# Performance work log

Measured on AMD Instinct MI355X. Metric: run time of the kernel, lower is better.

Reference implementation:

```python
import jax, jax.numpy as jnp
import numpy as np

# ---- constants from the module ----
E_L, E_e, E_i = -65.0, 0.0, -80.0
V_th, V_reset, V_floor = -50.0, -65.0, -200.0
dt = 0.25
T_STEPS = 4000
DECAY_AMPA = float(np.exp(-dt / 2.0))   # tau_ampa = 2.0
DECAY_GABA = float(np.exp(-dt / 9.0))   # tau_gaba = 9.0
C_M_E, G_L_E = 1.0, 1.0 / 20.0          # tau_m_E = 20
C_M_I, G_L_I = 0.5, 0.5 / 5.0           # tau_m_I = 5
REF_E = 12                               # round(3.0/0.25)
REF_I = 6                                # round(1.5/0.25)
CM_BACK = 80.0
SLOPE = 1.0                              # biophysical surrogate slope

@jax.custom_vjp
def spike(u):
    # Heaviside forward, fast-sigmoid surrogate backward (SurrogateSpike)
    return (u >= 0).astype(u.dtype)

def _spike_fwd(u):
    return (u >= 0).astype(u.dtype), u

def _spike_bwd(u, g):
    return (g * SLOPE / (1.0 + SLOPE * jnp.abs(u)) ** 2,)

spike.defvjp(_spike_fwd, _spike_bwd)

def _scale_grad(x, scale):
    # forward identity, gradient scaled by `scale`
    return x * scale + jax.lax.stop_gradient(x) * (1.0 - scale)

def lif_step(v, I_total, ref, C_m, g_L, ref_steps):
    dv = (dt / C_m) * (-g_L * (v - E_L) + I_total)
    dv = _scale_grad(dv, 1.0 / CM_BACK)
    v = jnp.maximum(v + dv, V_floor)
    ref = jnp.maximum(ref - 1, 0)
    can_spike = ref == 0
    s = spike(v - V_th) * can_spike.astype(v.dtype)
    spiked_or_ref = (s > 0) | ~can_spike
    v = jnp.where(spiked_or_ref, V_reset, v)
    ref = jnp.where(s > 0, ref_steps, ref)
    return v, s, ref

def setup_inputs() -> dict:
    key = jax.random.key(0)
    ks = jax.random.split(key, 6)
    T, B, N_IN, N_E, N_I, N_OUT = T_STEPS, 64, 64, 256, 64, 10

    def init_w(k, shape, mean, std):
        # init_weight: N(mean,std) clamped >=0, fan-in normalized
        w = jnp.maximum(jax.random.normal(k, shape, jnp.float32) * std + mean, 0.0)
        return w / shape[0]

    return {
        "input_spikes": (jax.random.uniform(ks[0], (T, B, N_IN)) < 0.02).astype(jnp.float32),
        "W_ff0": init_w(ks[1], (N_IN, N_E), 5.1, 3.8),
        "W_ff1": init_w(ks[2], (N_E, N_OUT), 5.1, 3.8),
        "W_ee": init_w(ks[3], (N_E, N_E), 0.0, 0.0),
        "W_ei": init_w(ks[4], (N_E, N_I), 1.0, 0.5),
        "W_ie": init_w(ks[5], (N_I, N_E), 3.0, 1.5),
    }

def reference(input_spikes, W_ff0, W_ff1, W_ee, W_ei, W_ie):
    # Dale's law: feedforward weights clamped >= 0 in forward
    W0 = jnp.maximum(W_ff0, 0.0)
    W1 = jnp.maximum(W_ff1, 0.0)
    B = input_spikes.shape[1]
    N_E, N_I, N_OUT = W0.shape[1], W_ei.shape[1], W1.shape[1]
    f32 = input_spikes.dtype

    z = lambda n: jnp.zeros((B, n), f32)
    vl = lambda n: jnp.full((B, n), E_L, f32)
    zr = lambda n: jnp.zeros((B, n), jnp.int32)

    carry0 = (vl(N_E), zr(N_E), z(N_E), z(N_E), z(N_E),   # E pop: v, ref, g_ampa, g_gaba, spikes
              vl(N_I), zr(N_I), z(N_I), z(N_I),           # I pop: v, ref, g_ampa, spikes
              vl(N_OUT), zr(N_OUT), z(N_OUT),             # out pop: v, ref, g_ampa
              z(N_OUT))                                    # output spike accumulator

    def step(c, s_in):
        v_e, r_e, ge_e, gi_e, s_e, v_i, r_i, ge_i, s_i, v_o, r_o, g_o, acc = c
        # exp_synapse: spike kicks first, then decay
        ge_e = (ge_e + s_in @ W0 + s_e @ W_ee) * DECAY_AMPA
        gi_e = (gi_e + s_i @ W_ie) * DECAY_GABA
        ge_i = (ge_i + s_e @ W_ei) * DECAY_AMPA
        # E neurons: COBA with excitation + inhibition
        v_e, s_e, r_e = lif_step(v_e, ge_e * (E_e - v_e) + gi_e * (E_i - v_e), r_e, C_M_E, G_L_E, REF_E)
        # I neurons: COBA excitation only
        v_i, s_i, r_i = lif_step(v_i, ge_i * (E_e - v_i), r_i, C_M_I, G_L_I, REF_I)
        # output layer driven by fresh E spikes
        g_o = (g_o + s_e @ W1) * DECAY_AMPA
        v_o, s_o, r_o = lif_step(v_o, g_o * (E_e - v_o), r_o, C_M_E, G_L_E, REF_E)
        acc = acc + s_o
        return (v_e, r_e, ge_e, gi_e, s_e, v_i, r_i, ge_i, s_i, v_o, r_o, g_o, acc), None

    cT, _ = jax.lax.scan(step, carry0, input_spikes)
    return cT[-1]  # [B, N_OUT] output spike counts over T_steps
```

## Files before the change

kernel.cpp:

```cpp
#include <hip/hip_runtime.h>
#include <math.h>

#pragma clang fp contract(off)

#define BB 64
#define N_IN 64
#define N_E 256
#define N_I 64
#define N_OUT 10

__device__ inline unsigned long long rfl64(unsigned long long x) {
  unsigned int lo = __builtin_amdgcn_readfirstlane((unsigned int)x);
  unsigned int hi = __builtin_amdgcn_readfirstlane((unsigned int)(x >> 32));
  return (((unsigned long long)hi) << 32) | (unsigned long long)lo;
}

__global__ __launch_bounds__(256, 1) void ping_kernel(
    const float* __restrict__ g_in,
    const float* __restrict__ g_W0,
    const float* __restrict__ g_W1,
    const float* __restrict__ g_Wee,
    const float* __restrict__ g_Wei,
    const float* __restrict__ g_Wie,
    float* __restrict__ g_out,
    int T, float dA, float dG)
{
  const int tid  = threadIdx.x;
  const int lane = tid & 63;
  const int wav  = tid >> 6;
  const int b    = blockIdx.x;
  const int col  = (lane < N_OUT) ? lane : 0;
  const int colO = 64 + col;

  __shared__ float sWie[N_I * N_E];
  __shared__ float sWeiO[N_E * 80];
  __shared__ float sZeroRow[256];
  __shared__ __align__(16) float sPK[2][64][4];
  __shared__ __align__(16) float sKoT[2][16][4];
  __shared__ __align__(16) unsigned sTag[2][4];
  __shared__ unsigned long long sME[2][4];
  __shared__ int sWee;

  {
    const float4* s0 = (const float4*)g_Wie; float4* d0 = (float4*)sWie;
    for (int k = tid; k < (N_I * N_E) / 4; k += 256) d0[k] = s0[k];
    {
      int j = tid;
      float* row = &sWeiO[j * 80];
      for (int c = 0; c < 64; ++c) row[c] = g_Wei[j * N_I + c];
      for (int o = 0; o < N_OUT; ++o) row[64 + o] = fmaxf(g_W1[j * N_OUT + o], 0.f);
      for (int c = 74; c < 80; ++c) row[c] = 0.f;
    }
  }
  sZeroRow[tid] = 0.f;
  if (tid < 4) { sME[0][tid] = 0ull; sME[1][tid] = 0ull; }
  if (tid < 8) sTag[tid >> 2][tid & 3] = 0u;
  if (tid == 0) sWee = 0;
  {
    bool any = false;
    const float4* p = (const float4*)g_Wee;
    for (int k = tid; k < (N_E * N_E) / 4; k += 256) {
      float4 x = p[k];
      any |= (x.x != 0.f) | (x.y != 0.f) | (x.z != 0.f) | (x.w != 0.f);
    }
    if (__ballot(any) != 0ull && lane == 0) sWee = 1;
  }
  __syncthreads();
  const int wee = sWee;

  float vE = -65.f, ge = 0.f, gi = 0.f; int rE = 0;
  float vI = -65.f, gI = 0.f; int rI = 0;
  float vO = -65.f, gO = 0.f, accO = 0.f; int rO = 0;

  unsigned long long mE = 0ull;
  unsigned long long mI = 0ull;

  float cur = g_in[b * N_IN + lane];
  float n1  = g_in[((T > 1 ? 1 : 0) * BB + b) * N_IN + lane];

  unsigned long long mInC = __ballot(cur != 0.f);
  unsigned long long aRemC = 0ull;
  bool vaC[4] = {false, false, false, false};
  float fwC[4];
  if (mInC) {
    unsigned long long a = mInC;
    int ja[4];
#pragma unroll
    for (int k = 0; k < 4; ++k) {
      vaC[k] = (a != 0ull); ja[k] = vaC[k] ? (__ffsll(a) - 1) : 0; a &= (a - 1ull);
    }
    aRemC = a;
#pragma unroll
    for (int k = 0; k < 4; ++k) fwC[k] = g_W0[ja[k] * N_E + tid];
  }

  const int base64 = wav * 64;

  if (!wee) {
    for (int t = 0; t < T; ++t) {
      const int slot = t & 1;
      const int tp = (t + 2 < T) ? (t + 2) : (T - 1);
      float n2 = g_in[(tp * BB + b) * N_IN + lane];

      float pEI = 0.f, kow = 0.f;
      {
        unsigned long long e = mE;
        while (e) {
          const float* qb[4];
#pragma unroll
          for (int k = 0; k < 4; ++k) {
            bool v = (e != 0ull); int j = v ? (__ffsll(e) - 1) : 0; e &= (e - 1ull);
            qb[k] = v ? &sWeiO[(base64 + j) * 80] : sZeroRow;
          }
          float fq[4], fr[4];
#pragma unroll
          for (int k = 0; k < 4; ++k) { fq[k] = qb[k][lane]; fr[k] = qb[k][colO]; }
#pragma unroll
          for (int k = 0; k < 4; ++k) pEI += fq[k];
#pragma unroll
          for (int k = 0; k < 4; ++k) kow += fr[k];
        }
      }

      sPK[slot][lane][wav] = pEI;
      if (lane < 16) sKoT[slot][lane][wav] = kow;
      asm volatile("" ::: "memory");
      if (lane == 0) *((volatile unsigned*)&sTag[slot][wav]) = (unsigned)(t + 1);

      unsigned long long pr0 = ((volatile unsigned long long*)&sTag[slot][0])[0];
      unsigned long long pr1 = ((volatile unsigned long long*)&sTag[slot][0])[1];

      float kie = 0.f;
      {
        unsigned long long c = mI;
        while (c) {
          const float* pb[8];
#pragma unroll
          for (int k = 0; k < 8; ++k) {
            bool v = (c != 0ull); int j = v ? (__ffsll(c) - 1) : 0; c &= (c - 1ull);
            pb[k] = v ? &sWie[j * N_E] : sZeroRow;
          }
          float fI[8];
#pragma unroll
          for (int k = 0; k < 8; ++k) fI[k] = pb[k][tid];
#pragma unroll
          for (int k = 0; k < 8; ++k) kie += fI[k];
        }
      }

      float kin = 0.f;
      if (mInC) {
#pragma unroll
        for (int k = 0; k < 4; ++k) kin += vaC[k] ? fmaxf(fwC[k], 0.f) : 0.f;
        while (aRemC) {
          int j = __ffsll(aRemC) - 1; aRemC &= (aRemC - 1ull);
          kin += fmaxf(g_W0[j * N_E + tid], 0.f);
        }
      }

      ge = (ge + kin) * dA;
      gi = (gi + kie) * dG;
      {
        float t2 = ge * (0.f - vE);
        float t3 = gi * (-80.f - vE);
        float Itot = t2 + t3;
        float dv = 0.25f * ((-0.05f) * (vE - (-65.f)) + Itot);
        dv = dv * 0.0125f + dv * 0.9875f;
        vE = fmaxf(vE + dv, -200.f);
        rE = rE - 1; if (rE < 0) rE = 0;
        bool can = (rE == 0);
        bool sE = ((vE - (-50.f)) >= 0.f) && can;
        vE = (sE || !can) ? -65.f : vE;
        rE = sE ? 12 : rE;
        mE = __ballot(sE);
      }

      mInC = __ballot(n1 != 0.f);
      aRemC = 0ull;
      vaC[0] = vaC[1] = vaC[2] = vaC[3] = false;
      if (mInC) {
        unsigned long long a = mInC;
        int ja[4];
#pragma unroll
        for (int k = 0; k < 4; ++k) {
          vaC[k] = (a != 0ull); ja[k] = vaC[k] ? (__ffsll(a) - 1) : 0; a &= (a - 1ull);
        }
        aRemC = a;
#pragma unroll
        for (int k = 0; k < 4; ++k) fwC[k] = g_W0[ja[k] * N_E + tid];
      }

      {
        const unsigned want = (unsigned)(t + 1);
        const unsigned long long want2 = (((unsigned long long)want) << 32) | want;
        if ((((pr0 ^ want2) | (pr1 ^ want2))) != 0ull) {
          volatile unsigned long long* vt = (volatile unsigned long long*)&sTag[slot][0];
          while (true) {
            unsigned long long a0 = vt[0], a1 = vt[1];
            if (((a0 ^ want2) | (a1 ^ want2)) == 0ull) break;
          }
        }
        asm volatile("" ::: "memory");
      }

      float4 P = *(const float4*)&sPK[slot][lane][0];
      float4 K = *(const float4*)&sKoT[slot][col][0];

      {
        float p = ((P.x + P.y) + P.z) + P.w;
        gI = (gI + p) * dA;
        float Ii = gI * (0.f - vI);
        float dvi = 0.5f * ((-0.1f) * (vI - (-65.f)) + Ii);
        dvi = dvi * 0.0125f + dvi * 0.9875f;
        vI = fmaxf(vI + dvi, -200.f);
        rI = rI - 1; if (rI < 0) rI = 0;
        bool canI = (rI == 0);
        bool sI = ((vI - (-50.f)) >= 0.f) && canI;
        vI = (sI || !canI) ? -65.f : vI;
        rI = sI ? 6 : rI;
        mI = __ballot(sI);
      }

      {
        float ko = ((K.x + K.y) + K.z) + K.w;
        gO = (gO + ko) * dA;
        float Io = gO * (0.f - vO);
        float dvo = 0.25f * ((-0.05f) * (vO - (-65.f)) + Io);
        dvo = dvo * 0.0125f + dvo * 0.9875f;
        vO = fmaxf(vO + dvo, -200.f);
        rO = rO - 1; if (rO < 0) rO = 0;
        bool canO = (rO == 0);
        bool sO = ((vO - (-50.f)) >= 0.f) && canO;
        vO = (sO || !canO) ? -65.f : vO;
        rO = sO ? 12 : rO;
        accO += sO ? 1.f : 0.f;
      }

      cur = n1; n1 = n2;
    }
  } else {
    unsigned long long we0 = 0ull, we1 = 0ull, we2 = 0ull, we3 = 0ull;
    for (int t = 0; t < T; ++t) {
      const int slot = t & 1;
      const int tp = (t + 2 < T) ? (t + 2) : (T - 1);
      float n2 = g_in[(tp * BB + b) * N_IN + lane];

      float pEI = 0.f, kow = 0.f;
      {
        unsigned long long e = mE;
        while (e) {
          const float* qb[4];
#pragma unroll
          for (int k = 0; k < 4; ++k) {
            bool v = (e != 0ull); int j = v ? (__ffsll(e) - 1) : 0; e &= (e - 1ull);
            qb[k] = v ? &sWeiO[(base64 + j) * 80] : sZeroRow;
          }
          float fq[4], fr[4];
#pragma unroll
          for (int k = 0; k < 4; ++k) { fq[k] = qb[k][lane]; fr[k] = qb[k][colO]; }
#pragma unroll
          for (int k = 0; k < 4; ++k) pEI += fq[k];
#pragma unroll
          for (int k = 0; k < 4; ++k) kow += fr[k];
        }
      }
      sPK[slot][lane][wav] = pEI;
      if (lane < 16) sKoT[slot][lane][wav] = kow;
      asm volatile("s_waitcnt lgkmcnt(0)" ::: "memory");
      if (lane == 0) *((volatile unsigned*)&sTag[slot][wav]) = (unsigned)(t + 1);

      float kie = 0.f;
      {
        unsigned long long c = mI;
        while (c) {
          const float* pb[8];
#pragma unroll
          for (int k = 0; k < 8; ++k) {
            bool v = (c != 0ull); int j = v ? (__ffsll(c) - 1) : 0; c &= (c - 1ull);
            pb[k] = v ? &sWie[j * N_E] : sZeroRow;
          }
          float fI[8];
#pragma unroll
          for (int k = 0; k < 8; ++k) fI[k] = pb[k][tid];
#pragma unroll
          for (int k = 0; k < 8; ++k) kie += fI[k];
        }
      }

      float kin = 0.f;
      if (mInC) {
#pragma unroll
        for (int k = 0; k < 4; ++k) kin += vaC[k] ? fmaxf(fwC[k], 0.f) : 0.f;
        while (aRemC) {
          int j = __ffsll(aRemC) - 1; aRemC &= (aRemC - 1ull);
          kin += fmaxf(g_W0[j * N_E + tid], 0.f);
        }
      }

      float kee = 0.f;
      {
        unsigned long long m0 = we0, m1 = we1, m2 = we2, m3 = we3;
        while (m0 | m1 | m2 | m3) {
          bool h0 = (m0 != 0ull), h1 = (m1 != 0ull), h2 = (m2 != 0ull), h3 = (m3 != 0ull);
          int idx = 0;
          if (h0)      { idx = __ffsll(m0) - 1;       m0 &= (m0 - 1ull); }
          else if (h1) { idx = 64 + __ffsll(m1) - 1;  m1 &= (m1 - 1ull); }
          else if (h2) { idx = 128 + __ffsll(m2) - 1; m2 &= (m2 - 1ull); }
          else if (h3) { idx = 192 + __ffsll(m3) - 1; m3 &= (m3 - 1ull); }
          kee += g_Wee[idx * N_E + tid];
        }
      }

      ge = ((ge + kin) + kee) * dA;
      gi = (gi + kie) * dG;
      {
        float t2 = ge * (0.f - vE);
        float t3 = gi * (-80.f - vE);
        float Itot = t2 + t3;
        float dv = 0.25f * ((-0.05f) * (vE - (-65.f)) + Itot);
        dv = dv * 0.0125f + dv * 0.9875f;
        vE = fmaxf(vE + dv, -200.f);
        rE = rE - 1; if (rE < 0) rE = 0;
        bool can = (rE == 0);
        bool sE = ((vE - (-50.f)) >= 0.f) && can;
        vE = (sE || !can) ? -65.f : vE;
        rE = sE ? 12 : rE;
        unsigned long long fresh = __ballot(sE);
        if (lane == 0) sME[slot][wav] = fresh;
        mE = fresh;
      }

      mInC = __ballot(n1 != 0.f);
      aRemC = 0ull;
      vaC[0] = vaC[1] = vaC[2] = vaC[3] = false;
      if (mInC) {
        unsigned long long a = mInC;
        int ja[4];
#pragma unroll
        for (int k = 0; k < 4; ++k) {
          vaC[k] = (a != 0ull); ja[k] = vaC[k] ? (__ffsll(a) - 1) : 0; a &= (a - 1ull);
        }
        aRemC = a;
#pragma unroll
        for (int k = 0; k < 4; ++k) fwC[k] = g_W0[ja[k] * N_E + tid];
      }

      {
        const unsigned want = (unsigned)(t + 1);
        const unsigned long long want2 = (((unsigned long long)want) << 32) | want;
        volatile unsigned long long* vt = (volatile unsigned long long*)&sTag[slot][0];
        while (true) {
          unsigned long long a0 = vt[0], a1 = vt[1];
          if (((a0 ^ want2) | (a1 ^ want2)) == 0ull) break;
        }
        asm volatile("" ::: "memory");
      }

      float4 P = *(const float4*)&sPK[slot][lane][0];
      float4 K = *(const float4*)&sKoT[slot][col][0];

      {
        float p = ((P.x + P.y) + P.z) + P.w;
        gI = (gI + p) * dA;
        float Ii = gI * (0.f - vI);
        float dvi = 0.5f * ((-0.1f) * (vI - (-65.f)) + Ii);
        dvi = dvi * 0.0125f + dvi * 0.9875f;
        vI = fmaxf(vI + dvi, -200.f);
        rI = rI - 1; if (rI < 0) rI = 0;
        bool canI = (rI == 0);
        bool sI = ((vI - (-50.f)) >= 0.f) && canI;
        vI = (sI || !canI) ? -65.f : vI;
        rI = sI ? 6 : rI;
        mI = __ballot(sI);
      }

      {
        float ko = ((K.x + K.y) + K.z) + K.w;
        gO = (gO + ko) * dA;
        float Io = gO * (0.f - vO);
        float dvo = 0.25f * ((-0.05f) * (vO - (-65.f)) + Io);
        dvo = dvo * 0.0125f + dvo * 0.9875f;
        vO = fmaxf(vO + dvo, -200.f);
        rO = rO - 1; if (rO < 0) rO = 0;
        bool canO = (rO == 0);
        bool sO = ((vO - (-50.f)) >= 0.f) && canO;
        vO = (sO || !canO) ? -65.f : vO;
        rO = sO ? 12 : rO;
        accO += sO ? 1.f : 0.f;
      }

      __syncthreads();
      we0 = rfl64(sME[slot][0]); we1 = rfl64(sME[slot][1]);
      we2 = rfl64(sME[slot][2]); we3 = rfl64(sME[slot][3]);

      cur = n1; n1 = n2;
    }
  }

  {
    float kd = 0.f;
    unsigned long long e = mE;
    while (e) {
      const float* rb[4];
#pragma unroll
      for (int k = 0; k < 4; ++k) {
        bool v = (e != 0ull); int j = v ? (__ffsll(e) - 1) : 0; e &= (e - 1ull);
        rb[k] = v ? &sWeiO[(base64 + j) * 80] : sZeroRow;
      }
      float fr[4];
#pragma unroll
      for (int k = 0; k < 4; ++k) fr[k] = rb[k][colO];
#pragma unroll
      for (int k = 0; k < 4; ++k) kd += fr[k];
    }
    __syncthreads();
    if (lane < 16) sKoT[0][lane][wav] = kd;
    __syncthreads();
    float4 K = *(const float4*)&sKoT[0][col][0];
    float ko = ((K.x + K.y) + K.z) + K.w;
    gO = (gO + ko) * dA;
    float Io = gO * (0.f - vO);
    float dvo = 0.25f * ((-0.05f) * (vO - (-65.f)) + Io);
    dvo = dvo * 0.0125f + dvo * 0.9875f;
    vO = fmaxf(vO + dvo, -200.f);
    rO = rO - 1; if (rO < 0) rO = 0;
    bool canO = (rO == 0);
    bool sO = ((vO - (-50.f)) >= 0.f) && canO;
    accO += sO ? 1.f : 0.f;
  }

  if (wav == 0 && lane < N_OUT) g_out[b * N_OUT + lane] = accO;
}

extern "C" void kernel_launch(void* const* d_in, const int* in_sizes, int n_in,
                              void* d_out, int out_size, void* d_ws, size_t ws_size,
                              hipStream_t stream) {
  const float* g_in  = (const float*)d_in[0];
  const float* g_W0  = (const float*)d_in[1];
  const float* g_W1  = (const float*)d_in[2];
  const float* g_Wee = (const float*)d_in[3];
  const float* g_Wei = (const float*)d_in[4];
  const float* g_Wie = (const float*)d_in[5];
  float* out = (float*)d_out;
  int T = in_sizes[0] / (BB * N_IN);
  float dA = (float)exp(-0.25 / 2.0);
  float dG = (float)exp(-0.25 / 9.0);
  ping_kernel<<<dim3(BB), dim3(256), 0, stream>>>(g_in, g_W0, g_W1, g_Wee, g_Wei, g_Wie, out, T, dA, dG);
}
```

Baseline: 4.770 ms.

## Add dedicated fifth wave for I/output populations to pipeline recurrence

Launches 320 threads and moves the inhibitory and output population updates (in the W_ee==0 path) onto a fifth wavefront. It exchanges spike masks with the four E-neuron waves through shared-memory tagged slots, so the E and I updates of consecutive timesteps can overlap instead of serializing in one wave. The change also widens the E-spike gather unroll from 4 to 8 and vectorizes the weight staging loads. The cost is extra spin-wait handshakes between waves and one more wave per block.

Result: no change. 4.745 ms (median of 2 runs) (-0.5%).

```diff
diff --git a/kernel.cpp b/kernel.cpp
--- a/kernel.cpp
+++ b/kernel.cpp
@@ -15,7 +15,7 @@
   return (((unsigned long long)hi) << 32) | (unsigned long long)lo;
 }
 
-__global__ __launch_bounds__(256, 1) void ping_kernel(
+__global__ __launch_bounds__(320, 1) void ping_kernel(
     const float* __restrict__ g_in,
     const float* __restrict__ g_W0,
     const float* __restrict__ g_W1,
@@ -31,6 +31,7 @@
   const int b    = blockIdx.x;
   const int col  = (lane < N_OUT) ? lane : 0;
   const int colO = 64 + col;
+  const int base64 = wav * 64;
 
   __shared__ float sWie[N_I * N_E];
   __shared__ float sWeiO[N_E * 80];
@@ -38,398 +39,468 @@
   __shared__ __align__(16) float sPK[2][64][4];
   __shared__ __align__(16) float sKoT[2][16][4];
   __shared__ __align__(16) unsigned sTag[2][4];
+  __shared__ __align__(8) unsigned long long sMI[2];
+  __shared__ unsigned sMITag[2];
   __shared__ unsigned long long sME[2][4];
   __shared__ int sWee;
 
   {
     const float4* s0 = (const float4*)g_Wie; float4* d0 = (float4*)sWie;
-    for (int k = tid; k < (N_I * N_E) / 4; k += 256) d0[k] = s0[k];
-    {
-      int j = tid;
-      float* row = &sWeiO[j * 80];
-      for (int c = 0; c < 64; ++c) row[c] = g_Wei[j * N_I + c];
-      for (int o = 0; o < N_OUT; ++o) row[64 + o] = fmaxf(g_W1[j * N_OUT + o], 0.f);
-      for (int c = 74; c < 80; ++c) row[c] = 0.f;
-    }
+    for (int k = tid; k < (N_I * N_E) / 4; k += 320) d0[k] = s0[k];
+    const float4* wei4 = (const float4*)g_Wei;
+    for (int k = tid; k < 256 * 16; k += 320) {
+      int r = k >> 4, c4 = k & 15;
+      *(float4*)&sWeiO[r * 80 + c4 * 4] = wei4[k];
+    }
+    for (int k = tid; k < 256 * N_OUT; k += 320) {
+      int r = k / N_OUT, o = k - r * N_OUT;
+      sWeiO[r * 80 + 64 + o] = fmaxf(g_W1[k], 0.f);
+    }
+    for (int k = tid; k < 256 * 6; k += 320) {
+      int r = k / 6, c = k - r * 6;
+      sWeiO[r * 80 + 74 + c] = 0.f;
+    }
+    for (int k = tid; k < 256; k += 320) sZeroRow[k] = 0.f;
   }
-  sZeroRow[tid] = 0.f;
-  if (tid < 4) { sME[0][tid] = 0ull; sME[1][tid] = 0ull; }
   if (tid < 8) sTag[tid >> 2][tid & 3] = 0u;
+  if (tid < 8) sME[tid >> 2][tid & 3] = 0ull;
+  if (tid < 2) { sMI[tid] = 0ull; sMITag[tid] = 0u; }
   if (tid == 0) sWee = 0;
+  __syncthreads();
   {
     bool any = false;
     const float4* p = (const float4*)g_Wee;
-    for (int k = tid; k < (N_E * N_E) / 4; k += 256) {
+    for (int k = tid; k < (N_E * N_E) / 4; k += 320) {
       float4 x = p[k];
       any |= (x.x != 0.f) | (x.y != 0.f) | (x.z != 0.f) | (x.w != 0.f);
     }
-    if (__ballot(any) != 0ull && lane == 0) sWee = 1;
+    if (any) sWee = 1;
   }
   __syncthreads();
   const int wee = sWee;
 
   float vE = -65.f, ge = 0.f, gi = 0.f; int rE = 0;
+  unsigned long long mE = 0ull;
   float vI = -65.f, gI = 0.f; int rI = 0;
+  unsigned long long mI = 0ull;
   float vO = -65.f, gO = 0.f, accO = 0.f; int rO = 0;
 
-  unsigned long long mE = 0ull;
-  unsigned long long mI = 0ull;
-
-  float cur = g_in[b * N_IN + lane];
-  float n1  = g_in[((T > 1 ? 1 : 0) * BB + b) * N_IN + lane];
-
-  unsigned long long mInC = __ballot(cur != 0.f);
-  unsigned long long aRemC = 0ull;
+  float cur = 0.f, n1 = 0.f;
+  unsigned long long mInC = 0ull, aRemC = 0ull;
   bool vaC[4] = {false, false, false, false};
   float fwC[4];
-  if (mInC) {
-    unsigned long long a = mInC;
-    int ja[4];
-#pragma unroll
-    for (int k = 0; k < 4; ++k) {
-      vaC[k] = (a != 0ull); ja[k] = vaC[k] ? (__ffsll(a) - 1) : 0; a &= (a - 1ull);
-    }
-    aRemC = a;
-#pragma unroll
-    for (int k = 0; k < 4; ++k) fwC[k] = g_W0[ja[k] * N_E + tid];
+  if (wav < 4) {
+    cur = g_in[b * N_IN + lane];
+    n1  = g_in[((T > 1 ? 1 : 0) * BB + b) * N_IN + lane];
+    mInC = __ballot(cur != 0.f);
+    if (mInC) {
+      unsigned long long a = mInC;
+      int ja[4];
+#pragma unroll
+      for (int k = 0; k < 4; ++k) {
+        vaC[k] = (a != 0ull); ja[k] = vaC[k] ? (__ffsll(a) - 1) : 0; a &= (a - 1ull);
+      }
+      aRemC = a;
+#pragma unroll
+      for (int k = 0; k < 4; ++k) fwC[k] = g_W0[ja[k] * N_E + tid];
+    }
   }
 
-  const int base64 = wav * 64;
-
-  if (!wee) {
-    for (int t = 0; t < T; ++t) {
-      const int slot = t & 1;
-      const int tp = (t + 2 < T) ? (t + 2) : (T - 1);
-      float n2 = g_in[(tp * BB + b) * N_IN + lane];
-
-      float pEI = 0.f, kow = 0.f;
-      {
-        unsigned long long e = mE;
-        while (e) {
-          const float* qb[4];
+  if (wav < 4) {
+    if (!wee) {
+      for (int t = 0; t < T; ++t) {
+        const int slot = t & 1;
+        const int slotP = (t + 1) & 1;
+        unsigned tgP = *((volatile unsigned*)&sMITag[slotP]);
+        unsigned long long mdP = *((volatile unsigned long long*)&sMI[slotP]);
+
+        const int tp = (t + 2 < T) ? (t + 2) : (T - 1);
+        float n2 = g_in[(tp * BB + b) * N_IN + lane];
+
+        float pEI = 0.f, kow = 0.f;
+        {
+          unsigned long long e = mE;
+          while (e) {
+            const float* qb[8];
+#pragma unroll
+            for (int k = 0; k < 8; ++k) {
+              bool v = (e != 0ull); int j = v ? (__ffsll(e) - 1) : 0; e &= (e - 1ull);
+              qb[k] = v ? &sWeiO[(base64 + j) * 80] : sZeroRow;
+            }
+            float fq[8], fr[8];
+#pragma unroll
+            for (int k = 0; k < 8; ++k) { fq[k] = qb[k][lane]; fr[k] = qb[k][colO]; }
+#pragma unroll
+            for (int k = 0; k < 8; ++k) pEI += fq[k];
+#pragma unroll
+            for (int k = 0; k < 8; ++k) kow += fr[k];
+          }
+        }
+
+        sPK[slot][lane][wav] = pEI;
+        if (lane < 16) sKoT[slot][lane][wav] = kow;
+        asm volatile("" ::: "memory");
+        if (lane == 0) *((volatile unsigned*)&sTag[slot][wav]) = (unsigned)(t + 1);
+
+        unsigned long long mIc;
+        if (tgP == (unsigned)t) {
+          mIc = mdP;
+        } else {
+          volatile unsigned* vt = (volatile unsigned*)&sMITag[slotP];
+          while (*vt != (unsigned)t) {}
+          asm volatile("" ::: "memory");
+          mIc = *((volatile unsigned long long*)&sMI[slotP]);
+        }
+
+        float kie = 0.f;
+        {
+          unsigned long long c = mIc;
+          while (c) {
+            const float* pb[8];
+#pragma unroll
+            for (int k = 0; k < 8; ++k) {
+              bool v = (c != 0ull); int j = v ? (__ffsll(c) - 1) : 0; c &= (c - 1ull);
+              pb[k] = v ? &sWie[j * N_E] : sZeroRow;
+            }
+            float fI[8];
+#pragma unroll
+            for (int k = 0; k < 8; ++k) fI[k] = pb[k][tid];
+#pragma unroll
+            for (int k = 0; k < 8; ++k) kie += fI[k];
+          }
+        }
+
+        float kin = 0.f;
+        if (mInC) {
+#pragma unroll
+          for (int k = 0; k < 4; ++k) kin += vaC[k] ? fmaxf(fwC[k], 0.f) : 0.f;
+          while (aRemC) {
+            int j = __ffsll(aRemC) - 1; aRemC &= (aRemC - 1ull);
+            kin += fmaxf(g_W0[j * N_E + tid], 0.f);
+          }
+        }
+
+        ge = (ge + kin) * dA;
+        gi = (gi + kie) * dG;
+        {
+          float t2 = ge * (0.f - vE);
+          float t3 = gi * (-80.f - vE);
+          float Itot = t2 + t3;
+          float dv = 0.25f * ((-0.05f) * (vE - (-65.f)) + Itot);
+          dv = dv * 0.0125f + dv * 0.9875f;
+          vE = fmaxf(vE + dv, -200.f);
+          rE = rE - 1; if (rE < 0) rE = 0;
+          bool can = (rE == 0);
+          bool sE = ((vE - (-50.f)) >= 0.f) && can;
+          vE = (sE || !can) ? -65.f : vE;
+          rE = sE ? 12 : rE;
+          mE = __ballot(sE);
+        }
+
+        mInC = __ballot(n1 != 0.f);
+        aRemC = 0ull;
+        vaC[0] = vaC[1] = vaC[2] = vaC[3] = false;
+        if (mInC) {
+          unsigned long long a = mInC;
+          int ja[4];
 #pragma unroll
           for (int k = 0; k < 4; ++k) {
-            bool v = (e != 0ull); int j = v ? (__ffsll(e) - 1) : 0; e &= (e - 1ull);
-            qb[k] = v ? &sWeiO[(base64 + j) * 80] : sZeroRow;
-          }
-          float fq[4], fr[4];
-#pragma unroll
-          for (int k = 0; k < 4; ++k) { fq[k] = qb[k][lane]; fr[k] = qb[k][colO]; }
-#pragma unroll
-          for (int k = 0; k < 4; ++k) pEI += fq[k];
-#pragma unroll
-          for (int k = 0; k < 4; ++k) kow += fr[k];
-        }
+            vaC[k] = (a != 0ull); ja[k] = vaC[k] ? (__ffsll(a) - 1) : 0; a &= (a - 1ull);
+          }
+          aRemC = a;
+#pragma unroll
+          for (int k = 0; k < 4; ++k) fwC[k] = g_W0[ja[k] * N_E + tid];
+        }
+
+        cur = n1; n1 = n2;
       }
-
-      sPK[slot][lane][wav] = pEI;
-      if (lane < 16) sKoT[slot][lane][wav] = kow;
-      asm volatile("" ::: "memory");
-      if (lane == 0) *((volatile unsigned*)&sTag[slot][wav]) = (unsigned)(t + 1);
-
-      unsigned long long pr0 = ((volatile unsigned long long*)&sTag[slot][0])[0];
-      unsigned long long pr1 = ((volatile unsigned long long*)&sTag[slot][0])[1];
-
-      float kie = 0.f;
-      {
-        unsigned long long c = mI;
-        while (c) {
-          const float* pb[8];
-#pragma unroll
-          for (int k = 0; k < 8; ++k) {
-            bool v = (c != 0ull); int j = v ? (__ffsll(c) - 1) : 0; c &= (c - 1ull);
-            pb[k] = v ? &sWie[j * N_E] : sZeroRow;
-          }
-          float fI[8];
-#pragma unroll
-          for (int k = 0; k < 8; ++k) fI[k] = pb[k][tid];
-#pragma unroll
-          for (int k = 0; k < 8; ++k) kie += fI[k];
-        }
-      }
-
-      float kin = 0.f;
-      if (mInC) {
-#pragma unroll
-        for (int k = 0; k < 4; ++k) kin += vaC[k] ? fmaxf(fwC[k], 0.f) : 0.f;
-        while (aRemC) {
-          int j = __ffsll(aRemC) - 1; aRemC &= (aRemC - 1ull);
-          kin += fmaxf(g_W0[j * N_E + tid], 0.f);
-        }
-      }
-
-      ge = (ge + kin) * dA;
-      gi = (gi + kie) * dG;
-      {
-        float t2 = ge * (0.f - vE);
-        float t3 = gi * (-80.f - vE);
-        float Itot = t2 + t3;
-        float dv = 0.25f * ((-0.05f) * (vE - (-65.f)) + Itot);
-        dv = dv * 0.0125f + dv * 0.9875f;
-        vE = fmaxf(vE + dv, -200.f);
-        rE = rE - 1; if (rE < 0) rE = 0;
-        bool can = (rE == 0);
-        bool sE = ((vE - (-50.f)) >= 0.f) && can;
-        vE = (sE || !can) ? -65.f : vE;
-        rE = sE ? 12 : rE;
-        mE = __ballot(sE);
-      }
-
-      mInC = __ballot(n1 != 0.f);
-      aRemC = 0ull;
-      vaC[0] = vaC[1] = vaC[2] = vaC[3] = false;
-      if (mInC) {
-        unsigned long long a = mInC;
-        int ja[4];
-#pragma unroll
-        for (int k = 0; k < 4; ++k) {
-          vaC[k] = (a != 0ull); ja[k] = vaC[k] ? (__ffsll(a) - 1) : 0; a &= (a - 1ull);
-        }
-        aRemC = a;
-#pragma unroll
-        for (int k = 0; k < 4; ++k) fwC[k] = g_W0[ja[k] * N_E + tid];
-      }
-
-      {
-        const unsigned want = (unsigned)(t + 1);
-        const unsigned long long want2 = (((unsigned long long)want) << 32) | want;
-        if ((((pr0 ^ want2) | (pr1 ^ want2))) != 0ull) {
+    } else {
+      unsigned long long we0 = 0ull, we1 = 0ull, we2 = 0ull, we3 = 0ull;
+      for (int t = 0; t < T; ++t) {
+        const int slot = t & 1;
+        const int tp = (t + 2 < T) ? (t + 2) : (T - 1);
+        float n2 = g_in[(tp * BB + b) * N_IN + lane];
+
+        float pEI = 0.f, kow = 0.f;
+        {
+          unsigned long long e = mE;
+          while (e) {
+            const float* qb[4];
+#pragma unroll
+            for (int k = 0; k < 4; ++k) {
+              bool v = (e != 0ull); int j = v ? (__ffsll(e) - 1) : 0; e &= (e - 1ull);
+              qb[k] = v ? &sWeiO[(base64 + j) * 80] : sZeroRow;
+            }
+            float fq[4], fr[4];
+#pragma unroll
+            for (int k = 0; k < 4; ++k) { fq[k] = qb[k][lane]; fr[k] = qb[k][colO]; }
+#pragma unroll
+            for (int k = 0; k < 4; ++k) pEI += fq[k];
+#pragma unroll
+            for (int k = 0; k < 4; ++k) kow += fr[k];
+          }
+        }
+        sPK[slot][lane][wav] = pEI;
+        if (lane < 16) sKoT[slot][lane][wav] = kow;
+        asm volatile("s_waitcnt lgkmcnt(0)" ::: "memory");
+        if (lane == 0) *((volatile unsigned*)&sTag[slot][wav]) = (unsigned)(t + 1);
+
+        float kie = 0.f;
+        {
+          unsigned long long c = mI;
+          while (c) {
+            const float* pb[8];
+#pragma unroll
+            for (int k = 0; k < 8; ++k) {
+              bool v = (c != 0ull); int j = v ? (__ffsll(c) - 1) : 0; c &= (c - 1ull);
+              pb[k] = v ? &sWie[j * N_E] : sZeroRow;
+            }
+            float fI[8];
+#pragma unroll
+            for (int k = 0; k < 8; ++k) fI[k] = pb[k][tid];
+#pragma unroll
+            for (int k = 0; k < 8; ++k) kie += fI[k];
+          }
+        }
+
+        float kin = 0.f;
+        if (mInC) {
+#pragma unroll
+          for (int k = 0; k < 4; ++k) kin += vaC[k] ? fmaxf(fwC[k], 0.f) : 0.f;
+          while (aRemC) {
+            int j = __ffsll(aRemC) - 1; aRemC &= (aRemC - 1ull);
+            kin += fmaxf(g_W0[j * N_E + tid], 0.f);
+          }
+        }
+
+        float kee = 0.f;
+        {
+          unsigned long long m0 = we0, m1 = we1, m2 = we2, m3 = we3;
+          while (m0 | m1 | m2 | m3) {
+            int idx = 0;
+            if (m0)      { idx = __ffsll(m0) - 1;       m0 &= (m0 - 1ull); }
+            else if (m1) { idx = 64 + __ffsll(m1) - 1;  m1 &= (m1 - 1ull); }
+            else if (m2) { idx = 128 + __ffsll(m2) - 1; m2 &= (m2 - 1ull); }
+            else         { idx = 192 + __ffsll(m3) - 1; m3 &= (m3 - 1ull); }
+            kee += g_Wee[idx * N_E + tid];
+          }
+        }
+
+        ge = ((ge + kin) + kee) * dA;
+        gi = (gi + kie) * dG;
+        {
+          float t2 = ge * (0.f - vE);
+          float t3 = gi * (-80.f - vE);
+          float Itot = t2 + t3;
+          float dv = 0.25f * ((-0.05f) * (vE - (-65.f)) + Itot);
+          dv = dv * 0.0125f + dv * 0.9875f;
+          vE = fmaxf(vE + dv, -200.f);
+          rE = rE - 1; if (rE < 0) rE = 0;
+          bool can = (rE == 0);
+          bool sE = ((vE - (-50.f)) >= 0.f) && can;
+          vE = (sE || !can) ? -65.f : vE;
+          rE = sE ? 12 : rE;
+          unsigned long long fresh = __ballot(sE);
+          if (lane == 0) sME[slot][wav] = fresh;
+          mE = fresh;
+        }
+
+        mInC = __ballot(n1 != 0.f);
+        aRemC = 0ull;
+        vaC[0] = vaC[1] = vaC[2] = vaC[3] = false;
+        if (mInC) {
+          unsigned long long a = mInC;
+          int ja[4];
+#pragma unroll
+          for (int k = 0; k < 4; ++k) {
+            vaC[k] = (a != 0ull); ja[k] = vaC[k] ? (__ffsll(a) - 1) : 0; a &= (a - 1ull);
+          }
+          aRemC = a;
+#pragma unroll
+          for (int k = 0; k < 4; ++k) fwC[k] = g_W0[ja[k] * N_E + tid];
+        }
+
+        {
+          const unsigned want = (unsigned)(t + 1);
+          const unsigned long long want2 = (((unsigned long long)want) << 32) | want;
           volatile unsigned long long* vt = (volatile unsigned long long*)&sTag[slot][0];
           while (true) {
             unsigned long long a0 = vt[0], a1 = vt[1];
             if (((a0 ^ want2) | (a1 ^ want2)) == 0ull) break;
           }
-        }
-        asm volatile("" ::: "memory");
+          asm volatile("" ::: "memory");
+        }
+
+        float4 P = *(const float4*)&sPK[slot][lane][0];
+        float4 K = *(const float4*)&sKoT[slot][col][0];
+
+        {
+          float p = ((P.x + P.y) + P.z) + P.w;
+          gI = (gI + p) * dA;
+          float Ii = gI * (0.f - vI);
+          float dvi = 0.5f * ((-0.1f) * (vI - (-65.f)) + Ii);
+          dvi = dvi * 0.0125f + dvi * 0.9875f;
+          vI = fmaxf(vI + dvi, -200.f);
+          rI = rI - 1; if (rI < 0) rI = 0;
+          bool canI = (rI == 0);
+          bool sI = ((vI - (-50.f)) >= 0.f) && canI;
+          vI = (sI || !canI) ? -65.f : vI;
+          rI = sI ? 6 : rI;
+          mI = __ballot(sI);
+        }
+
+        {
+          float ko = ((K.x + K.y) + K.z) + K.w;
+          gO = (gO + ko) * dA;
+          float Io = gO * (0.f - vO);
+          float dvo = 0.25f * ((-0.05f) * (vO - (-65.f)) + Io);
+          dvo = dvo * 0.0125f + dvo * 0.9875f;
+          vO = fmaxf(vO + dvo, -200.f);
+          rO = rO - 1; if (rO < 0) rO = 0;
+          bool canO = (rO == 0);
+          bool sO = ((vO - (-50.f)) >= 0.f) && canO;
+          vO = (sO || !canO) ? -65.f : vO;
+          rO = sO ? 12 : rO;
+          accO += sO ? 1.f : 0.f;
+        }
+
+        __syncthreads();
+        we0 = rfl64(sME[slot][0]); we1 = rfl64(sME[slot][1]);
+        we2 = rfl64(sME[slot][2]); we3 = rfl64(sME[slot][3]);
+
+        cur = n1; n1 = n2;
       }
-
-      float4 P = *(const float4*)&sPK[slot][lane][0];
-      float4 K = *(const float4*)&sKoT[slot][col][0];
-
-      {
-        float p = ((P.x + P.y) + P.z) + P.w;
-        gI = (gI + p) * dA;
-        float Ii = gI * (0.f - vI);
-        float dvi = 0.5f * ((-0.1f) * (vI - (-65.f)) + Ii);
-        dvi = dvi * 0.0125f + dvi * 0.9875f;
-        vI = fmaxf(vI + dvi, -200.f);
-        rI = rI - 1; if (rI < 0) rI = 0;
-        bool canI = (rI == 0);
-        bool sI = ((vI - (-50.f)) >= 0.f) && canI;
-        vI = (sI || !canI) ? -65.f : vI;
-        rI = sI ? 6 : rI;
-        mI = __ballot(sI);
+    }
+  } else {
+    if (!wee) {
+      for (int t = 0; t < T; ++t) {
+        const int slot = t & 1;
+        {
+          const unsigned want = (unsigned)(t + 1);
+          const unsigned long long want2 = (((unsigned long long)want) << 32) | want;
+          volatile unsigned long long* vt = (volatile unsigned long long*)&sTag[slot][0];
+          while (true) {
+            unsigned long long a0 = vt[0], a1 = vt[1];
+            if (((a0 ^ want2) | (a1 ^ want2)) == 0ull) break;
+          }
+          asm volatile("" ::: "memory");
+        }
+        float4 P = *(const float4*)&sPK[slot][lane][0];
+        float4 K = *(const float4*)&sKoT[slot][col][0];
+
+        unsigned long long mIv;
+        {
+          float p = ((P.x + P.y) + P.z) + P.w;
+          gI = (gI + p) * dA;
+          float Ii = gI * (0.f - vI);
+          float dvi = 0.5f * ((-0.1f) * (vI - (-65.f)) + Ii);
+          dvi = dvi * 0.0125f + dvi * 0.9875f;
+          vI = fmaxf(vI + dvi, -200.f);
+          rI = rI - 1; if (rI < 0) rI = 0;
+          bool canI = (rI == 0);
+          bool sI = ((vI - (-50.f)) >= 0.f) && canI;
+          vI = (sI || !canI) ? -65.f : vI;
+          rI = sI ? 6 : rI;
+          mIv = __ballot(sI);
+        }
+
+        {
+          float ko = ((K.x + K.y) + K.z) + K.w;
+          gO = (gO + ko) * dA;
+          float Io = gO * (0.f - vO);
+          float dvo = 0.25f * ((-0.05f) * (vO - (-65.f)) + Io);
+          dvo = dvo * 0.0125f + dvo * 0.9875f;
+          vO = fmaxf(vO + dvo, -200.f);
+          rO = rO - 1; if (rO < 0) rO = 0;
+          bool canO = (rO == 0);
+          bool sO = ((vO - (-50.f)) >= 0.f) && canO;
+          vO = (sO || !canO) ? -65.f : vO;
+          rO = sO ? 12 : rO;
+          accO += sO ? 1.f : 0.f;
+        }
+
+        if (lane == 0) {
+          sMI[slot] = mIv;
+          asm volatile("" ::: "memory");
+          *((volatile unsigned*)&sMITag[slot]) = (unsigned)(t + 1);
+        }
       }
-
-      {
-        float ko = ((K.x + K.y) + K.z) + K.w;
-        gO = (gO + ko) * dA;
-        float Io = gO * (0.f - vO);
-        float dvo = 0.25f * ((-0.05f) * (vO - (-65.f)) + Io);
-        dvo = dvo * 0.0125f + dvo * 0.9875f;
-        vO = fmaxf(vO + dvo, -200.f);
-        rO = rO - 1; if (rO < 0) rO = 0;
-        bool canO = (rO == 0);
-        bool sO = ((vO - (-50.f)) >= 0.f) && canO;
-        vO = (sO || !canO) ? -65.f : vO;
-        rO = sO ? 12 : rO;
-        accO += sO ? 1.f : 0.f;
+    } else {
+      for (int t = 0; t < T; ++t) __syncthreads();
+    }
+  }
+
+  if (!wee) {
+    float kd = 0.f;
+    if (wav < 4) {
+      unsigned long long e = mE;
+      while (e) {
+        const float* rb[8];
+#pragma unroll
+        for (int k = 0; k < 8; ++k) {
+          bool v = (e != 0ull); int j = v ? (__ffsll(e) - 1) : 0; e &= (e - 1ull);
+          rb[k] = v ? &sWeiO[(base64 + j) * 80] : sZeroRow;
+        }
+        float fr[8];
+#pragma unroll
+        for (int k = 0; k < 8; ++k) fr[k] = rb[k][colO];
+#pragma unroll
+        for (int k = 0; k < 8; ++k) kd += fr[k];
       }
-
-      cur = n1; n1 = n2;
+    }
+    __syncthreads();
+    if (wav < 4 && lane < 16) sKoT[0][lane][wav] = kd;
+    __syncthreads();
+    if (wav == 4) {
+      float4 K = *(const float4*)&sKoT[0][col][0];
+      float ko = ((K.x + K.y) + K.z) + K.w;
+      gO = (gO + ko) * dA;
+      float Io = gO * (0.f - vO);
+      float dvo = 0.25f * ((-0.05f) * (vO - (-65.f)) + Io);
+      dvo = dvo * 0.0125f + dvo * 0.9875f;
+      vO = fmaxf(vO + dvo, -200.f);
+      rO = rO - 1; if (rO < 0) rO = 0;
+      bool canO = (rO == 0);
+      bool sO = ((vO - (-50.f)) >= 0.f) && canO;
+      accO += sO ? 1.f : 0.f;
+      if (lane < N_OUT) g_out[b * N_OUT + lane] = accO;
     }
   } else {
-    unsigned long long we0 = 0ull, we1 = 0ull, we2 = 0ull, we3 = 0ull;
-    for (int t = 0; t < T; ++t) {
-      const int slot = t & 1;
-      const int tp = (t + 2 < T) ? (t + 2) : (T - 1);
-      float n2 = g_in[(tp * BB + b) * N_IN + lane];
-
-      float pEI = 0.f, kow = 0.f;
-      {
-        unsigned long long e = mE;
-        while (e) {
-          const float* qb[4];
-#pragma unroll
-          for (int k = 0; k < 4; ++k) {
-            bool v = (e != 0ull); int j = v ? (__ffsll(e) - 1) : 0; e &= (e - 1ull);
-            qb[k] = v ? &sWeiO[(base64 + j) * 80] : sZeroRow;
-          }
-          float fq[4], fr[4];
-#pragma unroll
-          for (int k = 0; k < 4; ++k) { fq[k] = qb[k][lane]; fr[k] = qb[k][colO]; }
-#pragma unroll
-          for (int k = 0; k < 4; ++k) pEI += fq[k];
-#pragma unroll
-          for (int k = 0; k < 4; ++k) kow += fr[k];
-        }
+    float kd = 0.f;
+    if (wav < 4) {
+      unsigned long long e = mE;
+      while (e) {
+        const float* rb[4];
+#pragma unroll
+        for (int k = 0; k < 4; ++k) {
+          bool v = (e != 0ull); int j = v ? (__ffsll(e) - 1) : 0; e &= (e - 1ull);
+          rb[k] = v ? &sWeiO[(base64 + j) * 80] : sZeroRow;
+        }
+        float fr[4];
+#pragma unroll
+        for (int k = 0; k < 4; ++k) fr[k] = rb[k][colO];
+#pragma unroll
+        for (int k = 0; k < 4; ++k) kd += fr[k];
       }
-      sPK[slot][lane][wav] = pEI;
-      if (lane < 16) sKoT[slot][lane][wav] = kow;
-      asm volatile("s_waitcnt lgkmcnt(0)" ::: "memory");
-      if (lane == 0) *((volatile unsigned*)&sTag[slot][wav]) = (unsigned)(t + 1);
-
-      float kie = 0.f;
-      {
-        unsigned long long c = mI;
-        while (c) {
-          const float* pb[8];
-#pragma unroll
-          for (int k = 0; k < 8; ++k) {
-            bool v = (c != 0ull); int j = v ? (__ffsll(c) - 1) : 0; c &= (c - 1ull);
-            pb[k] = v ? &sWie[j * N_E] : sZeroRow;
-          }
-          float fI[8];
-#pragma unroll
-          for (int k = 0; k < 8; ++k) fI[k] = pb[k][tid];
-#pragma unroll
-          for (int k = 0; k < 8; ++k) kie += fI[k];
-        }
-      }
-
-      float kin = 0.f;
-      if (mInC) {
-#pragma unroll
-        for (int k = 0; k < 4; ++k) kin += vaC[k] ? fmaxf(fwC[k], 0.f) : 0.f;
-        while (aRemC) {
-          int j = __ffsll(aRemC) - 1; aRemC &= (aRemC - 1ull);
-          kin += fmaxf(g_W0[j * N_E + tid], 0.f);
-        }
-      }
-
-      float kee = 0.f;
-      {
-        unsigned long long m0 = we0, m1 = we1, m2 = we2, m3 = we3;
-        while (m0 | m1 | m2 | m3) {
-          bool h0 = (m0 != 0ull), h1 = (m1 != 0ull), h2 = (m2 != 0ull), h3 = (m3 != 0ull);
-          int idx = 0;
-          if (h0)      { idx = __ffsll(m0) - 1;       m0 &= (m0 - 1ull); }
-          else if (h1) { idx = 64 + __ffsll(m1) - 1;  m1 &= (m1 - 1ull); }
-          else if (h2) { idx = 128 + __ffsll(m2) - 1; m2 &= (m2 - 1ull); }
-          else if (h3) { idx = 192 + __ffsll(m3) - 1; m3 &= (m3 - 1ull); }
-          kee += g_Wee[idx * N_E + tid];
-        }
-      }
-
-      ge = ((ge + kin) + kee) * dA;
-      gi = (gi + kie) * dG;
-      {
-        float t2 = ge * (0.f - vE);
-        float t3 = gi * (-80.f - vE);
-        float Itot = t2 + t3;
-        float dv = 0.25f * ((-0.05f) * (vE - (-65.f)) + Itot);
-        dv = dv * 0.0125f + dv * 0.9875f;
-        vE = fmaxf(vE + dv, -200.f);
-        rE = rE - 1; if (rE < 0) rE = 0;
-        bool can = (rE == 0);
-        bool sE = ((vE - (-50.f)) >= 0.f) && can;
-        vE = (sE || !can) ? -65.f : vE;
-        rE = sE ? 12 : rE;
-        unsigned long long fresh = __ballot(sE);
-        if (lane == 0) sME[slot][wav] = fresh;
-        mE = fresh;
-      }
-
-      mInC = __ballot(n1 != 0.f);
-      aRemC = 0ull;
-      vaC[0] = vaC[1] = vaC[2] = vaC[3] = false;
-      if (mInC) {
-        unsigned long long a = mInC;
-        int ja[4];
-#pragma unroll
-        for (int k = 0; k < 4; ++k) {
-          vaC[k] = (a != 0ull); ja[k] = vaC[k] ? (__ffsll(a) - 1) : 0; a &= (a - 1ull);
-        }
-        aRemC = a;
-#pragma unroll
-        for (int k = 0; k < 4; ++k) fwC[k] = g_W0[ja[k] * N_E + tid];
-      }
-
-      {
-        const unsigned want = (unsigned)(t + 1);
-        const unsigned long long want2 = (((unsigned long long)want) << 32) | want;
-        volatile unsigned long long* vt = (volatile unsigned long long*)&sTag[slot][0];
-        while (true) {
-          unsigned long long a0 = vt[0], a1 = vt[1];
-          if (((a0 ^ want2) | (a1 ^ want2)) == 0ull) break;
-        }
-        asm volatile("" ::: "memory");
-      }
-
-      float4 P = *(const float4*)&sPK[slot][lane][0];
-      float4 K = *(const float4*)&sKoT[slot][col][0];
-
-      {
-        float p = ((P.x + P.y) + P.z) + P.w;
-        gI = (gI + p) * dA;
-        float Ii = gI * (0.f - vI);
-        float dvi = 0.5f * ((-0.1f) * (vI - (-65.f)) + Ii);
-        dvi = dvi * 0.0125f + dvi * 0.9875f;
-        vI = fmaxf(vI + dvi, -200.f);
-        rI = rI - 1; if (rI < 0) rI = 0;
-        bool canI = (rI == 0);
-        bool sI = ((vI - (-50.f)) >= 0.f) && canI;
-        vI = (sI || !canI) ? -65.f : vI;
-        rI = sI ? 6 : rI;
-        mI = __ballot(sI);
-      }
-
-      {
-        float ko = ((K.x + K.y) + K.z) + K.w;
-        gO = (gO + ko) * dA;
-        float Io = gO * (0.f - vO);
-        float dvo = 0.25f * ((-0.05f) * (vO - (-65.f)) + Io);
-        dvo = dvo * 0.0125f + dvo * 0.9875f;
-        vO = fmaxf(vO + dvo, -200.f);
-        rO = rO - 1; if (rO < 0) rO = 0;
-        bool canO = (rO == 0);
-        bool sO = ((vO - (-50.f)) >= 0.f) && canO;
-        vO = (sO || !canO) ? -65.f : vO;
-        rO = sO ? 12 : rO;
-        accO += sO ? 1.f : 0.f;
-      }
-
-      __syncthreads();
-      we0 = rfl64(sME[slot][0]); we1 = rfl64(sME[slot][1]);
-      we2 = rfl64(sME[slot][2]); we3 = rfl64(sME[slot][3]);
-
-      cur = n1; n1 = n2;
+    }
+    __syncthreads();
+    if (wav < 4 && lane < 16) sKoT[0][lane][wav] = kd;
+    __syncthreads();
+    if (wav < 4) {
+      float4 K = *(const float4*)&sKoT[0][col][0];
+      float ko = ((K.x + K.y) + K.z) + K.w;
+      gO = (gO + ko) * dA;
+      float Io = gO * (0.f - vO);
+      float dvo = 0.25f * ((-0.05f) * (vO - (-65.f)) + Io);
+      dvo = dvo * 0.0125f + dvo * 0.9875f;
+      vO = fmaxf(vO + dvo, -200.f);
+      rO = rO - 1; if (rO < 0) rO = 0;
+      bool canO = (rO == 0);
+      bool sO = ((vO - (-50.f)) >= 0.f) && canO;
+      accO += sO ? 1.f : 0.f;
+      if (wav == 0 && lane < N_OUT) g_out[b * N_OUT + lane] = accO;
     }
   }
-
-  {
-    float kd = 0.f;
-    unsigned long long e = mE;
-    while (e) {
-      const float* rb[4];
-#pragma unroll
-      for (int k = 0; k < 4; ++k) {
-        bool v = (e != 0ull); int j = v ? (__ffsll(e) - 1) : 0; e &= (e - 1ull);
-        rb[k] = v ? &sWeiO[(base64 + j) * 80] : sZeroRow;
-      }
-      float fr[4];
-#pragma unroll
-      for (int k = 0; k < 4; ++k) fr[k] = rb[k][colO];
-#pragma unroll
-      for (int k = 0; k < 4; ++k) kd += fr[k];
-    }
-    __syncthreads();
-    if (lane < 16) sKoT[0][lane][wav] = kd;
-    __syncthreads();
-    float4 K = *(const float4*)&sKoT[0][col][0];
-    float ko = ((K.x + K.y) + K.z) + K.w;
-    gO = (gO + ko) * dA;
-    float Io = gO * (0.f - vO);
-    float dvo = 0.25f * ((-0.05f) * (vO - (-65.f)) + Io);
-    dvo = dvo * 0.0125f + dvo * 0.9875f;
-    vO = fmaxf(vO + dvo, -200.f);
-    rO = rO - 1; if (rO < 0) rO = 0;
-    bool canO = (rO == 0);
-    bool sO = ((vO - (-50.f)) >= 0.f) && canO;
-    accO += sO ? 1.f : 0.f;
-  }
-
-  if (wav == 0 && lane < N_OUT) g_out[b * N_OUT + lane] = accO;
 }
 
 extern "C" void kernel_launch(void* const* d_in, const int* in_sizes, int n_in,
@@ -445,5 +516,5 @@
   int T = in_sizes[0] / (BB * N_IN);
   float dA = (float)exp(-0.25 / 2.0);
   float dG = (float)exp(-0.25 / 9.0);
-  ping_kernel<<<dim3(BB), dim3(256), 0, stream>>>(g_in, g_W0, g_W1, g_Wee, g_Wei, g_Wie, out, T, dA, dG);
+  ping_kernel<<<dim3(BB), dim3(320), 0, stream>>>(g_in, g_W0, g_W1, g_Wee, g_Wei, g_Wie, out, T, dA, dG);
 }
```
